# Performance work log

Hardware: AMD Instinct MI355X
Metric: run time of the kernel (lower is better)

## Reference

```python
import jax, jax.numpy as jnp
import numpy as np
import math

D_MODEL = 768
N_HEADS = 12
D_HEAD = D_MODEL // N_HEADS
B, T = 2, 2048


def setup_inputs() -> dict:
    key = jax.random.key(0)
    ks = jax.random.split(key, 12)
    s = 1.0 / math.sqrt(D_MODEL)
    inp = {
        'x': jax.random.normal(ks[0], (B, T, D_MODEL), dtype=jnp.float32),
        'gates': jax.random.uniform(ks[1], (B, N_HEADS), dtype=jnp.float32),
        'Wq': jax.random.normal(ks[2], (D_MODEL, D_MODEL), dtype=jnp.float32) * s,
        'bq': jnp.zeros((D_MODEL,), dtype=jnp.float32),
        'Wk': jax.random.normal(ks[3], (D_MODEL, D_MODEL), dtype=jnp.float32) * s,
        'bk': jnp.zeros((D_MODEL,), dtype=jnp.float32),
        'Wv': jax.random.normal(ks[4], (D_MODEL, D_MODEL), dtype=jnp.float32) * s,
        'bv': jnp.zeros((D_MODEL,), dtype=jnp.float32),
        'Wo': jax.random.normal(ks[5], (D_MODEL, D_MODEL), dtype=jnp.float32) * s,
        'bo': jnp.zeros((D_MODEL,), dtype=jnp.float32),
    }
    return inp


def reference(x, gates, Wq, bq, Wk, bk, Wv, bv, Wo, bo):
    Bs, Ts, D = x.shape
    H, Dh = N_HEADS, D_HEAD
    # Linear layers use W stored as [out,in] in torch; here weights are [in,out].
    q = (x @ Wq + bq).reshape(Bs, Ts, H, Dh)
    k = (x @ Wk + bk).reshape(Bs, Ts, H, Dh)
    v = (x @ Wv + bv).reshape(Bs, Ts, H, Dh)
    scores = jnp.einsum('bthd,bshd->bhts', q, k) / math.sqrt(Dh)
    A = jax.nn.softmax(scores, axis=-1)
    # post-softmax per-head gating
    A = A * gates[:, :, None, None]
    z = jnp.einsum('bhts,bshd->bthd', A, v).reshape(Bs, Ts, D)
    out = z @ Wo + bo
    return out, A
```

## Files before the change

### kernel.cpp

```cpp
#include <hip/hip_runtime.h>
#include <hip/hip_bf16.h>
#include <stdint.h>

#define D_MODEL 768
#define NH 12
#define DH 64
#define BB 2
#define TT 2048
#define BT (BB*TT)

typedef unsigned short u16;
typedef __attribute__((ext_vector_type(8))) short short8;
typedef __attribute__((ext_vector_type(4))) float f32x4;

__device__ __forceinline__ u16 f2bf(float f) {
  union { float f; unsigned int u; } c; c.f = f;
  unsigned int u = c.u;
  u += 0x7fff + ((u >> 16) & 1);
  return (u16)(u >> 16);
}

__device__ __forceinline__ void gload_lds16(const void* g, void* l) {
  __builtin_amdgcn_global_load_lds(
      (const __attribute__((address_space(1))) void*)g,
      (__attribute__((address_space(3))) void*)l, 16, 0, 0);
}

__global__ void k_convert_x(const float* __restrict__ in, u16* __restrict__ out, int n4) {
  int i = blockIdx.x * blockDim.x + threadIdx.x;
  if (i >= n4) return;
  float4 v = ((const float4*)in)[i];
  unsigned int p0 = (unsigned int)f2bf(v.x) | ((unsigned int)f2bf(v.y) << 16);
  unsigned int p1 = (unsigned int)f2bf(v.z) | ((unsigned int)f2bf(v.w) << 16);
  ((uint2*)out)[i] = make_uint2(p0, p1);
}

__global__ void k_transpose_bf16(const float* __restrict__ in, u16* __restrict__ out, int R, int C) {
  __shared__ float tile[32][33];
  int bc = blockIdx.x * 32;
  int br = blockIdx.y * 32;
  int tx = threadIdx.x, ty = threadIdx.y;
  #pragma unroll
  for (int i = 0; i < 32; i += 8)
    tile[ty + i][tx] = in[(size_t)(br + ty + i) * C + bc + tx];
  __syncthreads();
  #pragma unroll
  for (int i = 0; i < 32; i += 8)
    out[(size_t)(bc + ty + i) * R + br + tx] = f2bf(tile[tx][ty + i]);
}

template<int MODE>
__global__ __launch_bounds__(256, 2)
void k_gemm(const u16* __restrict__ Abf, const u16* __restrict__ Bt,
            const float* __restrict__ bias0, const float* __restrict__ bias1,
            const float* __restrict__ bias2,
            u16* __restrict__ q_buf, u16* __restrict__ k_buf, u16* __restrict__ vt_buf,
            float* __restrict__ out, int K) {
  __shared__ u16 As[128 * 32];
  __shared__ u16 Bs[128 * 32];
  int tid = threadIdx.x;
  int lane = tid & 63, w = tid >> 6;
  int ln = lane & 15, lg = lane >> 4;
  int wm = w >> 1, wn = w & 1;
  int m0 = blockIdx.y * 128, n0 = blockIdx.x * 128;
  f32x4 acc[4][4] = {};
  int c0 = tid, c1 = tid + 256;

  for (int kb = 0; kb < K; kb += 32) {
    gload_lds16(Abf + (size_t)(m0 + (c0 >> 2)) * K + kb + (c0 & 3) * 8, (char*)As + c0 * 16);
    gload_lds16(Abf + (size_t)(m0 + (c1 >> 2)) * K + kb + (c1 & 3) * 8, (char*)As + c1 * 16);
    gload_lds16(Bt  + (size_t)(n0 + (c0 >> 2)) * K + kb + (c0 & 3) * 8, (char*)Bs + c0 * 16);
    gload_lds16(Bt  + (size_t)(n0 + (c1 >> 2)) * K + kb + (c1 & 3) * 8, (char*)Bs + c1 * 16);
    __syncthreads();
    short8 af[4], bfr[4];
    #pragma unroll
    for (int mt = 0; mt < 4; ++mt)
      af[mt] = *(const short8*)&As[(wm * 64 + mt * 16 + ln) * 32 + lg * 8];
    #pragma unroll
    for (int nt = 0; nt < 4; ++nt)
      bfr[nt] = *(const short8*)&Bs[(wn * 64 + nt * 16 + ln) * 32 + lg * 8];
    #pragma unroll
    for (int mt = 0; mt < 4; ++mt)
      #pragma unroll
      for (int nt = 0; nt < 4; ++nt)
        acc[mt][nt] = __builtin_amdgcn_mfma_f32_16x16x32_bf16(af[mt], bfr[nt], acc[mt][nt], 0, 0, 0);
    __syncthreads();
  }

  #pragma unroll
  for (int mt = 0; mt < 4; ++mt) {
    #pragma unroll
    for (int nt = 0; nt < 4; ++nt) {
      #pragma unroll
      for (int r = 0; r < 4; ++r) {
        int row = m0 + wm * 64 + mt * 16 + lg * 4 + r;
        int col = n0 + wn * 64 + nt * 16 + ln;
        float v = acc[mt][nt][r];
        if (MODE == 0) {
          int b = row >> 11, t = row & 2047;
          if (col < 768) {
            v += bias0[col];
            int h = col >> 6, d = col & 63;
            q_buf[(((size_t)b * NH + h) * TT + t) * DH + d] = f2bf(v);
          } else if (col < 1536) {
            int c2 = col - 768; v += bias1[c2];
            int h = c2 >> 6, d = c2 & 63;
            k_buf[(((size_t)b * NH + h) * TT + t) * DH + d] = f2bf(v);
          } else {
            int c2 = col - 1536; v += bias2[c2];
            int h = c2 >> 6, d = c2 & 63;
            vt_buf[(((size_t)b * NH + h) * DH + d) * TT + t] = f2bf(v);
          }
        } else {
          out[(size_t)row * 768 + col] = v + bias0[col];
        }
      }
    }
  }
}

__global__ __launch_bounds__(256, 2)
void k_attn(const u16* __restrict__ Q, const u16* __restrict__ Kb,
            const u16* __restrict__ Vt, const float* __restrict__ gates,
            float* __restrict__ A_out, u16* __restrict__ z_buf) {
  int bh = blockIdx.y;
  int b = bh / NH, h = bh % NH;
  int q0 = blockIdx.x * 16;
  int tid = threadIdx.x;
  int lane = tid & 63, w = tid >> 6;
  int ln = lane & 15, lg = lane >> 4;
  const u16* Qbh = Q  + (size_t)bh * TT * DH;
  const u16* Kbh = Kb + (size_t)bh * TT * DH;
  const u16* Vbh = Vt + (size_t)bh * DH * TT;
  float gate = gates[bh];

  short8 qf0 = *(const short8*)&Qbh[(size_t)(q0 + ln) * DH + lg * 8];
  short8 qf1 = *(const short8*)&Qbh[(size_t)(q0 + ln) * DH + 32 + lg * 8];

  int key_base = w * 512;
  f32x4 sacc[32];
  #pragma unroll
  for (int t = 0; t < 32; ++t) {
    const u16* kp = &Kbh[(size_t)(key_base + t * 16 + ln) * DH + lg * 8];
    short8 kf0 = *(const short8*)kp;
    short8 kf1 = *(const short8*)(kp + 32);
    f32x4 c = {0.f, 0.f, 0.f, 0.f};
    c = __builtin_amdgcn_mfma_f32_16x16x32_bf16(qf0, kf0, c, 0, 0, 0);
    c = __builtin_amdgcn_mfma_f32_16x16x32_bf16(qf1, kf1, c, 0, 0, 0);
    sacc[t] = c;
  }

  __shared__ float red_m[4][16];
  __shared__ float red_s[4][16];

  float mr[4];
  #pragma unroll
  for (int r = 0; r < 4; ++r) {
    float m = sacc[0][r];
    #pragma unroll
    for (int t = 1; t < 32; ++t) m = fmaxf(m, sacc[t][r]);
    #pragma unroll
    for (int mk = 1; mk <= 8; mk <<= 1) m = fmaxf(m, __shfl_xor(m, mk, 64));
    mr[r] = m;
  }
  if (ln == 0) {
    #pragma unroll
    for (int r = 0; r < 4; ++r) red_m[w][lg * 4 + r] = mr[r];
  }
  __syncthreads();
  float gm[4];
  #pragma unroll
  for (int r = 0; r < 4; ++r) {
    int q = lg * 4 + r;
    gm[r] = fmaxf(fmaxf(red_m[0][q], red_m[1][q]), fmaxf(red_m[2][q], red_m[3][q]));
  }

  const float cs = 0.18033688011112042f;
  float sr[4] = {0.f, 0.f, 0.f, 0.f};
  #pragma unroll
  for (int t = 0; t < 32; ++t) {
    #pragma unroll
    for (int r = 0; r < 4; ++r) {
      float e = exp2f((sacc[t][r] - gm[r]) * cs);
      sacc[t][r] = e;
      sr[r] += e;
    }
  }
  #pragma unroll
  for (int r = 0; r < 4; ++r) {
    #pragma unroll
    for (int mk = 1; mk <= 8; mk <<= 1) sr[r] += __shfl_xor(sr[r], mk, 64);
  }
  if (ln == 0) {
    #pragma unroll
    for (int r = 0; r < 4; ++r) red_s[w][lg * 4 + r] = sr[r];
  }
  __syncthreads();
  float scale[4];
  #pragma unroll
  for (int r = 0; r < 4; ++r) {
    int q = lg * 4 + r;
    float denom = red_s[0][q] + red_s[1][q] + red_s[2][q] + red_s[3][q];
    scale[r] = gate / denom;
  }

  float* Arow = A_out + ((size_t)bh * TT + q0) * TT;
  __shared__ u16 P_lds[4][16][136];
  f32x4 zacc[4] = {};
  #pragma unroll
  for (int ch = 0; ch < 4; ++ch) {
    #pragma unroll
    for (int tt = 0; tt < 8; ++tt) {
      int t = ch * 8 + tt;
      int key = key_base + t * 16 + ln;
      #pragma unroll
      for (int r = 0; r < 4; ++r) {
        float p = sacc[t][r] * scale[r];
        Arow[(size_t)(lg * 4 + r) * TT + key] = p;
        P_lds[w][lg * 4 + r][tt * 16 + ln] = f2bf(p);
      }
    }
    #pragma unroll
    for (int ks = 0; ks < 4; ++ks) {
      short8 pf = *(const short8*)&P_lds[w][ln][ks * 32 + lg * 8];
      #pragma unroll
      for (int dt = 0; dt < 4; ++dt) {
        const u16* vp = &Vbh[(size_t)(dt * 16 + ln) * TT + key_base + ch * 128 + ks * 32 + lg * 8];
        short8 vf = *(const short8*)vp;
        zacc[dt] = __builtin_amdgcn_mfma_f32_16x16x32_bf16(pf, vf, zacc[dt], 0, 0, 0);
      }
    }
  }

  __shared__ float Zred[4][16][64];
  #pragma unroll
  for (int dt = 0; dt < 4; ++dt)
    #pragma unroll
    for (int r = 0; r < 4; ++r)
      Zred[w][lg * 4 + r][dt * 16 + ln] = zacc[dt][r];
  __syncthreads();
  {
    int d = lane;
    #pragma unroll
    for (int i = 0; i < 4; ++i) {
      int qq = w + i * 4;
      float s = Zred[0][qq][d] + Zred[1][qq][d] + Zred[2][qq][d] + Zred[3][qq][d];
      z_buf[((size_t)b * TT + q0 + qq) * D_MODEL + h * DH + d] = f2bf(s);
    }
  }
}

extern "C" void kernel_launch(void* const* d_in, const int* in_sizes, int n_in,
                              void* d_out, int out_size, void* d_ws, size_t ws_size,
                              hipStream_t stream) {
  const float* x     = (const float*)d_in[0];
  const float* gates = (const float*)d_in[1];
  const float* Wq    = (const float*)d_in[2];
  const float* bq    = (const float*)d_in[3];
  const float* Wk    = (const float*)d_in[4];
  const float* bk    = (const float*)d_in[5];
  const float* Wv    = (const float*)d_in[6];
  const float* bv    = (const float*)d_in[7];
  const float* Wo    = (const float*)d_in[8];
  const float* bo    = (const float*)d_in[9];
  float* out   = (float*)d_out;
  float* A_out = out + (size_t)BT * D_MODEL;

  char* ws = (char*)d_ws;
  u16* x_bf   = (u16*)ws; ws += (size_t)BT * D_MODEL * 2;
  u16* wqkvT  = (u16*)ws; ws += (size_t)3 * D_MODEL * D_MODEL * 2;
  u16* woT    = (u16*)ws; ws += (size_t)D_MODEL * D_MODEL * 2;
  u16* q_buf  = (u16*)ws; ws += (size_t)BT * D_MODEL * 2;
  u16* k_buf  = (u16*)ws; ws += (size_t)BT * D_MODEL * 2;
  u16* vt_buf = (u16*)ws; ws += (size_t)BT * D_MODEL * 2;
  u16* z_buf  = (u16*)ws; ws += (size_t)BT * D_MODEL * 2;

  k_convert_x<<<(BT * D_MODEL / 4 + 255) / 256, 256, 0, stream>>>(x, x_bf, BT * D_MODEL / 4);
  dim3 tb(32, 8);
  dim3 tg(D_MODEL / 32, D_MODEL / 32);
  k_transpose_bf16<<<tg, tb, 0, stream>>>(Wq, wqkvT, D_MODEL, D_MODEL);
  k_transpose_bf16<<<tg, tb, 0, stream>>>(Wk, wqkvT + (size_t)D_MODEL * D_MODEL, D_MODEL, D_MODEL);
  k_transpose_bf16<<<tg, tb, 0, stream>>>(Wv, wqkvT + (size_t)2 * D_MODEL * D_MODEL, D_MODEL, D_MODEL);
  k_transpose_bf16<<<tg, tb, 0, stream>>>(Wo, woT, D_MODEL, D_MODEL);

  k_gemm<0><<<dim3(2304 / 128, BT / 128), 256, 0, stream>>>(
      x_bf, wqkvT, bq, bk, bv, q_buf, k_buf, vt_buf, nullptr, D_MODEL);

  k_attn<<<dim3(TT / 16, BB * NH), 256, 0, stream>>>(q_buf, k_buf, vt_buf, gates, A_out, z_buf);

  k_gemm<1><<<dim3(D_MODEL / 128, BT / 128), 256, 0, stream>>>(
      z_buf, woT, bo, nullptr, nullptr, nullptr, nullptr, nullptr, out, D_MODEL);
}
```

Measured before the change: 317.0 us.

## Use 8 waves with fp16-packed scores and coalesced LDS-staged attention stores

Splits each query tile's keys across 8 waves of 256 keys instead of 4 waves of 512. Raw scores and exponentials are held as packed fp16 pairs to cut register pressure, so occupancy can rise. The attention-probability output is now written from the bf16 tile already staged in LDS, as coalesced row-contiguous nontemporal float2 stores, instead of strided per-lane scalar stores. The P and Z shared buffers are unioned to save LDS. The trade-off is that the stored A values carry fp16/bf16 rounding rather than fp32 precision, which could affect accuracy checks.

```diff
diff --git a/kernel.cpp b/kernel.cpp
--- a/kernel.cpp
+++ b/kernel.cpp
@@ -8,16 +8,25 @@
 #define BB 2
 #define TT 2048
 #define BT (BB*TT)
+#define NW 8
+#define KPW 256
 
 typedef unsigned short u16;
 typedef __attribute__((ext_vector_type(8))) short short8;
 typedef __attribute__((ext_vector_type(4))) float f32x4;
+typedef __attribute__((ext_vector_type(2))) float f32x2;
+typedef __attribute__((ext_vector_type(2))) __fp16 half2v;
 
 __device__ __forceinline__ u16 f2bf(float f) {
   union { float f; unsigned int u; } c; c.f = f;
   unsigned int u = c.u;
   u += 0x7fff + ((u >> 16) & 1);
   return (u16)(u >> 16);
+}
+
+__device__ __forceinline__ float bf2f(u16 b) {
+  union { unsigned int u; float f; } c; c.u = ((unsigned int)b) << 16;
+  return c.f;
 }
 
 __device__ __forceinline__ void gload_lds16(const void* g, void* l) {
@@ -119,7 +128,12 @@
   }
 }
 
-__global__ __launch_bounds__(256, 2)
+union AttnSM {
+  u16  P[NW][16][136];
+  float Z[NW][16][72];
+};
+
+__global__ __launch_bounds__(512, 4)
 void k_attn(const u16* __restrict__ Q, const u16* __restrict__ Kb,
             const u16* __restrict__ Vt, const float* __restrict__ gates,
             float* __restrict__ A_out, u16* __restrict__ z_buf) {
@@ -134,63 +148,67 @@
   const u16* Vbh = Vt + (size_t)bh * DH * TT;
   float gate = gates[bh];
 
+  __shared__ float red_m[NW][16];
+  __shared__ float red_s[NW][16];
+  __shared__ AttnSM sm;
+
   short8 qf0 = *(const short8*)&Qbh[(size_t)(q0 + ln) * DH + lg * 8];
   short8 qf1 = *(const short8*)&Qbh[(size_t)(q0 + ln) * DH + 32 + lg * 8];
 
-  int key_base = w * 512;
-  f32x4 sacc[32];
-  #pragma unroll
-  for (int t = 0; t < 32; ++t) {
-    const u16* kp = &Kbh[(size_t)(key_base + t * 16 + ln) * DH + lg * 8];
+  int base = w * KPW;
+
+  half2v sh[16][2];
+  float m[4] = {-1e30f, -1e30f, -1e30f, -1e30f};
+  #pragma unroll
+  for (int t = 0; t < 16; ++t) {
+    const u16* kp = &Kbh[(size_t)(base + t * 16 + ln) * DH + lg * 8];
     short8 kf0 = *(const short8*)kp;
     short8 kf1 = *(const short8*)(kp + 32);
     f32x4 c = {0.f, 0.f, 0.f, 0.f};
     c = __builtin_amdgcn_mfma_f32_16x16x32_bf16(qf0, kf0, c, 0, 0, 0);
     c = __builtin_amdgcn_mfma_f32_16x16x32_bf16(qf1, kf1, c, 0, 0, 0);
-    sacc[t] = c;
-  }
-
-  __shared__ float red_m[4][16];
-  __shared__ float red_s[4][16];
-
-  float mr[4];
-  #pragma unroll
-  for (int r = 0; r < 4; ++r) {
-    float m = sacc[0][r];
-    #pragma unroll
-    for (int t = 1; t < 32; ++t) m = fmaxf(m, sacc[t][r]);
-    #pragma unroll
-    for (int mk = 1; mk <= 8; mk <<= 1) m = fmaxf(m, __shfl_xor(m, mk, 64));
-    mr[r] = m;
-  }
+    sh[t][0] = __builtin_amdgcn_cvt_pkrtz(c[0], c[1]);
+    sh[t][1] = __builtin_amdgcn_cvt_pkrtz(c[2], c[3]);
+    m[0] = fmaxf(m[0], c[0]); m[1] = fmaxf(m[1], c[1]);
+    m[2] = fmaxf(m[2], c[2]); m[3] = fmaxf(m[3], c[3]);
+  }
+
+  #pragma unroll
+  for (int r = 0; r < 4; ++r)
+    #pragma unroll
+    for (int mk = 1; mk <= 8; mk <<= 1) m[r] = fmaxf(m[r], __shfl_xor(m[r], mk, 64));
   if (ln == 0) {
     #pragma unroll
-    for (int r = 0; r < 4; ++r) red_m[w][lg * 4 + r] = mr[r];
+    for (int r = 0; r < 4; ++r) red_m[w][lg * 4 + r] = m[r];
   }
   __syncthreads();
   float gm[4];
   #pragma unroll
   for (int r = 0; r < 4; ++r) {
     int q = lg * 4 + r;
-    gm[r] = fmaxf(fmaxf(red_m[0][q], red_m[1][q]), fmaxf(red_m[2][q], red_m[3][q]));
+    float v = red_m[0][q];
+    #pragma unroll
+    for (int i = 1; i < NW; ++i) v = fmaxf(v, red_m[i][q]);
+    gm[r] = v;
   }
 
   const float cs = 0.18033688011112042f;
   float sr[4] = {0.f, 0.f, 0.f, 0.f};
   #pragma unroll
-  for (int t = 0; t < 32; ++t) {
-    #pragma unroll
-    for (int r = 0; r < 4; ++r) {
-      float e = exp2f((sacc[t][r] - gm[r]) * cs);
-      sacc[t][r] = e;
-      sr[r] += e;
-    }
-  }
-  #pragma unroll
-  for (int r = 0; r < 4; ++r) {
+  for (int t = 0; t < 16; ++t) {
+    #pragma unroll
+    for (int j = 0; j < 2; ++j) {
+      float s0 = (float)sh[t][j][0], s1 = (float)sh[t][j][1];
+      float e0 = exp2f((s0 - gm[j * 2]) * cs);
+      float e1 = exp2f((s1 - gm[j * 2 + 1]) * cs);
+      sh[t][j] = __builtin_amdgcn_cvt_pkrtz(e0, e1);
+      sr[j * 2] += e0; sr[j * 2 + 1] += e1;
+    }
+  }
+  #pragma unroll
+  for (int r = 0; r < 4; ++r)
     #pragma unroll
     for (int mk = 1; mk <= 8; mk <<= 1) sr[r] += __shfl_xor(sr[r], mk, 64);
-  }
   if (ln == 0) {
     #pragma unroll
     for (int r = 0; r < 4; ++r) red_s[w][lg * 4 + r] = sr[r];
@@ -200,51 +218,61 @@
   #pragma unroll
   for (int r = 0; r < 4; ++r) {
     int q = lg * 4 + r;
-    float denom = red_s[0][q] + red_s[1][q] + red_s[2][q] + red_s[3][q];
+    float denom = red_s[0][q];
+    #pragma unroll
+    for (int i = 1; i < NW; ++i) denom += red_s[i][q];
     scale[r] = gate / denom;
   }
 
   float* Arow = A_out + ((size_t)bh * TT + q0) * TT;
-  __shared__ u16 P_lds[4][16][136];
   f32x4 zacc[4] = {};
   #pragma unroll
-  for (int ch = 0; ch < 4; ++ch) {
+  for (int ch = 0; ch < 2; ++ch) {
     #pragma unroll
     for (int tt = 0; tt < 8; ++tt) {
       int t = ch * 8 + tt;
-      int key = key_base + t * 16 + ln;
       #pragma unroll
       for (int r = 0; r < 4; ++r) {
-        float p = sacc[t][r] * scale[r];
-        Arow[(size_t)(lg * 4 + r) * TT + key] = p;
-        P_lds[w][lg * 4 + r][tt * 16 + ln] = f2bf(p);
+        float p = (float)sh[t][r >> 1][r & 1] * scale[r];
+        sm.P[w][lg * 4 + r][tt * 16 + ln] = f2bf(p);
       }
     }
     #pragma unroll
     for (int ks = 0; ks < 4; ++ks) {
-      short8 pf = *(const short8*)&P_lds[w][ln][ks * 32 + lg * 8];
+      short8 pf = *(const short8*)&sm.P[w][ln][ks * 32 + lg * 8];
       #pragma unroll
       for (int dt = 0; dt < 4; ++dt) {
-        const u16* vp = &Vbh[(size_t)(dt * 16 + ln) * TT + key_base + ch * 128 + ks * 32 + lg * 8];
+        const u16* vp = &Vbh[(size_t)(dt * 16 + ln) * TT + base + ch * 128 + ks * 32 + lg * 8];
         short8 vf = *(const short8*)vp;
         zacc[dt] = __builtin_amdgcn_mfma_f32_16x16x32_bf16(pf, vf, zacc[dt], 0, 0, 0);
       }
     }
-  }
-
-  __shared__ float Zred[4][16][64];
+    #pragma unroll
+    for (int row = 0; row < 16; ++row) {
+      unsigned int pk = *(const unsigned int*)&sm.P[w][row][lane * 2];
+      f32x2 v2;
+      v2.x = bf2f((u16)pk);
+      v2.y = bf2f((u16)(pk >> 16));
+      __builtin_nontemporal_store(v2,
+          (f32x2*)&Arow[(size_t)row * TT + base + ch * 128 + lane * 2]);
+    }
+  }
+
+  __syncthreads();
   #pragma unroll
   for (int dt = 0; dt < 4; ++dt)
     #pragma unroll
     for (int r = 0; r < 4; ++r)
-      Zred[w][lg * 4 + r][dt * 16 + ln] = zacc[dt][r];
+      sm.Z[w][lg * 4 + r][dt * 16 + ln] = zacc[dt][r];
   __syncthreads();
   {
     int d = lane;
     #pragma unroll
-    for (int i = 0; i < 4; ++i) {
-      int qq = w + i * 4;
-      float s = Zred[0][qq][d] + Zred[1][qq][d] + Zred[2][qq][d] + Zred[3][qq][d];
+    for (int i = 0; i < 2; ++i) {
+      int qq = w + i * 8;
+      float s = 0.f;
+      #pragma unroll
+      for (int j = 0; j < NW; ++j) s += sm.Z[j][qq][d];
       z_buf[((size_t)b * TT + q0 + qq) * D_MODEL + h * DH + d] = f2bf(s);
     }
   }
@@ -286,7 +314,7 @@
   k_gemm<0><<<dim3(2304 / 128, BT / 128), 256, 0, stream>>>(
       x_bf, wqkvT, bq, bk, bv, q_buf, k_buf, vt_buf, nullptr, D_MODEL);
 
-  k_attn<<<dim3(TT / 16, BB * NH), 256, 0, stream>>>(q_buf, k_buf, vt_buf, gates, A_out, z_buf);
+  k_attn<<<dim3(TT / 16, BB * NH), 512, 0, stream>>>(q_buf, k_buf, vt_buf, gates, A_out, z_buf);
 
   k_gemm<1><<<dim3(D_MODEL / 128, BT / 128), 256, 0, stream>>>(
       z_buf, woT, bo, nullptr, nullptr, nullptr, nullptr, nullptr, out, D_MODEL);
```

Measured after the change: 283.8 us. 1.12x faster.

## Restructure attention into per-wave two-pass softmax with coalesced nontemporal A stores

Applied to the files above, without the earlier changes.

Each wave now owns 16 query rows across all keys. A first pass computes exp scores, the row sums and the unnormalized P·V. A second pass recomputes QK^T, normalizes, stages the rows in LDS and writes A with wide coalesced nontemporal stores. This drops the 32-tile score array held in registers, the cross-wave reductions, syncs and the Z reduction, and uses smaller 128-thread blocks for higher occupancy. The cost is doubling the QK^T MFMA work and K loads. It also removes the max subtraction, which risks overflow for large scores.

```diff
diff --git a/kernel.cpp b/kernel.cpp
--- a/kernel.cpp
+++ b/kernel.cpp
@@ -12,6 +12,7 @@
 typedef unsigned short u16;
 typedef __attribute__((ext_vector_type(8))) short short8;
 typedef __attribute__((ext_vector_type(4))) float f32x4;
+typedef __attribute__((ext_vector_type(2))) float f32x2;
 
 __device__ __forceinline__ u16 f2bf(float f) {
   union { float f; unsigned int u; } c; c.f = f;
@@ -119,133 +120,98 @@
   }
 }
 
-__global__ __launch_bounds__(256, 2)
+union WaveSM {
+  u16   p16[16][136];
+  float p32[16][132];
+};
+
+__global__ __launch_bounds__(128, 4)
 void k_attn(const u16* __restrict__ Q, const u16* __restrict__ Kb,
             const u16* __restrict__ Vt, const float* __restrict__ gates,
             float* __restrict__ A_out, u16* __restrict__ z_buf) {
   int bh = blockIdx.y;
   int b = bh / NH, h = bh % NH;
-  int q0 = blockIdx.x * 16;
   int tid = threadIdx.x;
   int lane = tid & 63, w = tid >> 6;
   int ln = lane & 15, lg = lane >> 4;
+  int q0 = blockIdx.x * 32 + w * 16;
   const u16* Qbh = Q  + (size_t)bh * TT * DH;
   const u16* Kbh = Kb + (size_t)bh * TT * DH;
   const u16* Vbh = Vt + (size_t)bh * DH * TT;
   float gate = gates[bh];
 
+  __shared__ WaveSM sm[2];
+  WaveSM& ws = sm[w];
+
   short8 qf0 = *(const short8*)&Qbh[(size_t)(q0 + ln) * DH + lg * 8];
   short8 qf1 = *(const short8*)&Qbh[(size_t)(q0 + ln) * DH + 32 + lg * 8];
 
-  int key_base = w * 512;
-  f32x4 sacc[32];
-  #pragma unroll
-  for (int t = 0; t < 32; ++t) {
-    const u16* kp = &Kbh[(size_t)(key_base + t * 16 + ln) * DH + lg * 8];
-    short8 kf0 = *(const short8*)kp;
-    short8 kf1 = *(const short8*)(kp + 32);
-    f32x4 c = {0.f, 0.f, 0.f, 0.f};
-    c = __builtin_amdgcn_mfma_f32_16x16x32_bf16(qf0, kf0, c, 0, 0, 0);
-    c = __builtin_amdgcn_mfma_f32_16x16x32_bf16(qf1, kf1, c, 0, 0, 0);
-    sacc[t] = c;
-  }
-
-  __shared__ float red_m[4][16];
-  __shared__ float red_s[4][16];
-
-  float mr[4];
-  #pragma unroll
-  for (int r = 0; r < 4; ++r) {
-    float m = sacc[0][r];
-    #pragma unroll
-    for (int t = 1; t < 32; ++t) m = fmaxf(m, sacc[t][r]);
-    #pragma unroll
-    for (int mk = 1; mk <= 8; mk <<= 1) m = fmaxf(m, __shfl_xor(m, mk, 64));
-    mr[r] = m;
-  }
-  if (ln == 0) {
-    #pragma unroll
-    for (int r = 0; r < 4; ++r) red_m[w][lg * 4 + r] = mr[r];
-  }
-  __syncthreads();
-  float gm[4];
-  #pragma unroll
-  for (int r = 0; r < 4; ++r) {
-    int q = lg * 4 + r;
-    gm[r] = fmaxf(fmaxf(red_m[0][q], red_m[1][q]), fmaxf(red_m[2][q], red_m[3][q]));
-  }
-
   const float cs = 0.18033688011112042f;
-  float sr[4] = {0.f, 0.f, 0.f, 0.f};
-  #pragma unroll
-  for (int t = 0; t < 32; ++t) {
-    #pragma unroll
-    for (int r = 0; r < 4; ++r) {
-      float e = exp2f((sacc[t][r] - gm[r]) * cs);
-      sacc[t][r] = e;
-      sr[r] += e;
-    }
-  }
-  #pragma unroll
-  for (int r = 0; r < 4; ++r) {
-    #pragma unroll
-    for (int mk = 1; mk <= 8; mk <<= 1) sr[r] += __shfl_xor(sr[r], mk, 64);
-  }
-  if (ln == 0) {
-    #pragma unroll
-    for (int r = 0; r < 4; ++r) red_s[w][lg * 4 + r] = sr[r];
-  }
-  __syncthreads();
-  float scale[4];
-  #pragma unroll
-  for (int r = 0; r < 4; ++r) {
-    int q = lg * 4 + r;
-    float denom = red_s[0][q] + red_s[1][q] + red_s[2][q] + red_s[3][q];
-    scale[r] = gate / denom;
-  }
-
-  float* Arow = A_out + ((size_t)bh * TT + q0) * TT;
-  __shared__ u16 P_lds[4][16][136];
+
   f32x4 zacc[4] = {};
-  #pragma unroll
-  for (int ch = 0; ch < 4; ++ch) {
+  float l[4] = {0.f, 0.f, 0.f, 0.f};
+  for (int ch = 0; ch < 16; ++ch) {
     #pragma unroll
     for (int tt = 0; tt < 8; ++tt) {
-      int t = ch * 8 + tt;
-      int key = key_base + t * 16 + ln;
+      const u16* kp = &Kbh[(size_t)(ch * 128 + tt * 16 + ln) * DH + lg * 8];
+      short8 kf0 = *(const short8*)kp;
+      short8 kf1 = *(const short8*)(kp + 32);
+      f32x4 c = {0.f, 0.f, 0.f, 0.f};
+      c = __builtin_amdgcn_mfma_f32_16x16x32_bf16(qf0, kf0, c, 0, 0, 0);
+      c = __builtin_amdgcn_mfma_f32_16x16x32_bf16(qf1, kf1, c, 0, 0, 0);
       #pragma unroll
       for (int r = 0; r < 4; ++r) {
-        float p = sacc[t][r] * scale[r];
-        Arow[(size_t)(lg * 4 + r) * TT + key] = p;
-        P_lds[w][lg * 4 + r][tt * 16 + ln] = f2bf(p);
+        float e = __builtin_amdgcn_exp2f(c[r] * cs);
+        l[r] += e;
+        ws.p16[lg * 4 + r][tt * 16 + ln] = f2bf(e);
       }
     }
     #pragma unroll
     for (int ks = 0; ks < 4; ++ks) {
-      short8 pf = *(const short8*)&P_lds[w][ln][ks * 32 + lg * 8];
+      short8 pf = *(const short8*)&ws.p16[ln][ks * 32 + lg * 8];
       #pragma unroll
       for (int dt = 0; dt < 4; ++dt) {
-        const u16* vp = &Vbh[(size_t)(dt * 16 + ln) * TT + key_base + ch * 128 + ks * 32 + lg * 8];
+        const u16* vp = &Vbh[(size_t)(dt * 16 + ln) * TT + ch * 128 + ks * 32 + lg * 8];
         short8 vf = *(const short8*)vp;
         zacc[dt] = __builtin_amdgcn_mfma_f32_16x16x32_bf16(pf, vf, zacc[dt], 0, 0, 0);
       }
     }
   }
 
-  __shared__ float Zred[4][16][64];
+  #pragma unroll
+  for (int r = 0; r < 4; ++r)
+    #pragma unroll
+    for (int mk = 1; mk <= 8; mk <<= 1) l[r] += __shfl_xor(l[r], mk, 64);
+  float scale[4];
+  #pragma unroll
+  for (int r = 0; r < 4; ++r) scale[r] = gate / l[r];
+
   #pragma unroll
   for (int dt = 0; dt < 4; ++dt)
     #pragma unroll
     for (int r = 0; r < 4; ++r)
-      Zred[w][lg * 4 + r][dt * 16 + ln] = zacc[dt][r];
-  __syncthreads();
-  {
-    int d = lane;
-    #pragma unroll
-    for (int i = 0; i < 4; ++i) {
-      int qq = w + i * 4;
-      float s = Zred[0][qq][d] + Zred[1][qq][d] + Zred[2][qq][d] + Zred[3][qq][d];
-      z_buf[((size_t)b * TT + q0 + qq) * D_MODEL + h * DH + d] = f2bf(s);
+      z_buf[((size_t)b * TT + q0 + lg * 4 + r) * D_MODEL + h * DH + dt * 16 + ln] =
+          f2bf(zacc[dt][r] * scale[r]);
+
+  float* Arow = A_out + ((size_t)bh * TT + q0) * TT;
+  for (int ch = 0; ch < 16; ++ch) {
+    #pragma unroll
+    for (int tt = 0; tt < 8; ++tt) {
+      const u16* kp = &Kbh[(size_t)(ch * 128 + tt * 16 + ln) * DH + lg * 8];
+      short8 kf0 = *(const short8*)kp;
+      short8 kf1 = *(const short8*)(kp + 32);
+      f32x4 c = {0.f, 0.f, 0.f, 0.f};
+      c = __builtin_amdgcn_mfma_f32_16x16x32_bf16(qf0, kf0, c, 0, 0, 0);
+      c = __builtin_amdgcn_mfma_f32_16x16x32_bf16(qf1, kf1, c, 0, 0, 0);
+      #pragma unroll
+      for (int r = 0; r < 4; ++r)
+        ws.p32[lg * 4 + r][tt * 16 + ln] = __builtin_amdgcn_exp2f(c[r] * cs) * scale[r];
+    }
+    #pragma unroll
+    for (int row = 0; row < 16; ++row) {
+      f32x2 v2 = *(const f32x2*)&ws.p32[row][lane * 2];
+      __builtin_nontemporal_store(v2,
+          (f32x2*)&Arow[(size_t)row * TT + ch * 128 + lane * 2]);
     }
   }
 }
@@ -286,7 +252,7 @@
   k_gemm<0><<<dim3(2304 / 128, BT / 128), 256, 0, stream>>>(
       x_bf, wqkvT, bq, bk, bv, q_buf, k_buf, vt_buf, nullptr, D_MODEL);
 
-  k_attn<<<dim3(TT / 16, BB * NH), 256, 0, stream>>>(q_buf, k_buf, vt_buf, gates, A_out, z_buf);
+  k_attn<<<dim3(TT / 32, BB * NH), 128, 0, stream>>>(q_buf, k_buf, vt_buf, gates, A_out, z_buf);
 
   k_gemm<1><<<dim3(D_MODEL / 128, BT / 128), 256, 0, stream>>>(
       z_buf, woT, bo, nullptr, nullptr, nullptr, nullptr, nullptr, out, D_MODEL);
```

Result: slower. 350.1 us (+10.4%).
